# Kernel optimization log

Measured on AMD Instinct MI355X. Metric: run time of the kernel, lower is better.

## Reference

```python
import jax, jax.numpy as jnp
import numpy as np
from jax import lax

V, H, L, F = 50304, 512, 6, 2048
SKIP_INTERVAL = 1
B, S = 4, 1024


def layer_norm(x, w, b, eps=1e-5):
    mu = jnp.mean(x, axis=-1, keepdims=True)
    var = jnp.mean(jnp.square(x - mu), axis=-1, keepdims=True)
    return (x - mu) * lax.rsqrt(var + eps) * w + b


def setup_inputs() -> dict:
    key = jax.random.key(0)
    ks = jax.random.split(key, 8)
    s = 0.02
    return {
        "input_ids": jax.random.randint(ks[0], (B, S), 0, V, dtype=jnp.int64),
        "embed_in": jax.random.normal(ks[1], (V, H), jnp.float32) * s,
        "hp_w": jax.random.normal(ks[2], (H, H), jnp.float32) * s,
        "hp_b": jnp.zeros((H,), jnp.float32),
        "ln_w": jnp.ones((L, H), jnp.float32),
        "ln_b": jnp.zeros((L, H), jnp.float32),
        "W1": jax.random.normal(ks[3], (L, H, F), jnp.float32) * s,
        "b1": jnp.zeros((L, F), jnp.float32),
        "W2": jax.random.normal(ks[4], (L, F, H), jnp.float32) * s,
        "b2": jnp.zeros((L, H), jnp.float32),
        "ln_f_w": jnp.ones((H,), jnp.float32),
        "ln_f_b": jnp.zeros((H,), jnp.float32),
        "embed_out_w": jax.random.normal(ks[5], (V, H), jnp.float32) * s,
    }


def _stack(h, ln_w, ln_b, W1, b1, W2, b2):
    # scan over L layers; each is pre-LN residual MLP: h + gelu(LN(h) @ W1 + b1) @ W2 + b2
    def step(h, p):
        lw, lb, w1, bb1, w2, bb2 = p
        y = layer_norm(h, lw, lb)
        h = h + jnp.dot(jax.nn.gelu(jnp.dot(y, w1) + bb1), w2) + bb2
        return h, None
    h, _ = lax.scan(step, h, (ln_w, ln_b, W1, b1, W2, b2))
    return h


def reference(input_ids, embed_in, hp_w, hp_b, ln_w, ln_b, W1, b1, W2, b2, ln_f_w, ln_f_b, embed_out_w):
    # forward_selective with attention_mask=None and stateless layers is
    # position-independent, so the token loop vectorizes exactly to [B,S,H].
    h = embed_in[input_ids]  # [B,S,H] gather
    h = _stack(h, ln_w, ln_b, W1, b1, W2, b2)
    for _ in range(SKIP_INTERVAL):
        h = jnp.dot(h, hp_w.T) + hp_b  # hidden_proj
        h = _stack(h, ln_w, ln_b, W1, b1, W2, b2)
    normed = layer_norm(h, ln_f_w, ln_f_b)
    logits = jnp.dot(normed, embed_out_w.T)  # [B,S,V]
    final_hidden = h[:, -1, :]  # [B,H]
    return logits, final_hidden
```

## Files before the change

### kernel.cpp

```cpp
#include <hip/hip_runtime.h>
#include <hip/hip_bf16.h>
#include <cstdint>

using bf16 = __hip_bfloat16;
typedef __bf16 bf16x8 __attribute__((ext_vector_type(8)));
typedef float f32x4 __attribute__((ext_vector_type(4)));

constexpr int Hd = 512;
constexpr int Ld = 6;
constexpr int Fd = 2048;
constexpr int Vd = 50304;
constexpr int Vpad = 50432;
constexpr int Md = 4096;

__device__ __forceinline__ unsigned short f2b(float x) {
  return __builtin_bit_cast(unsigned short, __float2bfloat16(x));
}

__device__ __forceinline__ float gelu_tanh(float x) {
  const float c = 0.7978845608028654f;
  float x3 = x * x * x;
  return 0.5f * x * (1.0f + tanhf(c * (x + 0.044715f * x3)));
}

__device__ __forceinline__ void load16_lds(const bf16* g, bf16* l) {
  __builtin_amdgcn_global_load_lds(
      (const __attribute__((address_space(1))) void*)g,
      (__attribute__((address_space(3))) void*)l, 16, 0, 0);
}

__global__ __launch_bounds__(256) void cast8(const float* __restrict__ in,
                                             bf16* __restrict__ out, int n8) {
  int i = blockIdx.x * 256 + threadIdx.x;
  if (i >= n8) return;
  const float4* p = (const float4*)in;
  float4 a = p[2 * i], b = p[2 * i + 1];
  uint4 o = {(unsigned)f2b(a.x) | ((unsigned)f2b(a.y) << 16),
             (unsigned)f2b(a.z) | ((unsigned)f2b(a.w) << 16),
             (unsigned)f2b(b.x) | ((unsigned)f2b(b.y) << 16),
             (unsigned)f2b(b.z) | ((unsigned)f2b(b.w) << 16)};
  ((uint4*)out)[i] = o;
}

__global__ __launch_bounds__(256) void zero16(bf16* __restrict__ p, int n8) {
  int i = blockIdx.x * 256 + threadIdx.x;
  if (i < n8) ((uint4*)p)[i] = uint4{0, 0, 0, 0};
}

__global__ void transpose_cast(const float* __restrict__ in, bf16* __restrict__ out,
                               int R, int C) {
  __shared__ float tile[32][33];
  int l = blockIdx.z;
  in += (size_t)l * R * C;
  out += (size_t)l * R * C;
  int c0 = blockIdx.x * 32, r0 = blockIdx.y * 32;
#pragma unroll
  for (int i = 0; i < 4; i++) {
    int r = r0 + threadIdx.y + i * 8;
    tile[threadIdx.y + i * 8][threadIdx.x] = in[(size_t)r * C + c0 + threadIdx.x];
  }
  __syncthreads();
#pragma unroll
  for (int i = 0; i < 4; i++) {
    int c = c0 + threadIdx.y + i * 8;
    out[(size_t)c * R + r0 + threadIdx.x] = (bf16)tile[threadIdx.x][threadIdx.y + i * 8];
  }
}

__global__ void gather_embed(const int* __restrict__ ids, const float* __restrict__ emb,
                             float* __restrict__ h) {
  int row = blockIdx.x;
  int id = ids[row];
  const float4* src = (const float4*)(emb + (size_t)id * Hd);
  float4* dst = (float4*)(h + (size_t)row * Hd);
  dst[threadIdx.x] = src[threadIdx.x];
}

template <int MODE>
__global__ __launch_bounds__(256) void ln_rows(
    const float* __restrict__ h, const float* __restrict__ p0,
    const float* __restrict__ p1, const float* __restrict__ fb,
    const float* __restrict__ w, const float* __restrict__ b,
    float* __restrict__ hout, bf16* __restrict__ y) {
  int row = blockIdx.x * 4 + (threadIdx.x >> 6);
  int lane = threadIdx.x & 63;
  size_t base = (size_t)row * Hd + lane * 8;
  float xv[8];
  if constexpr (MODE == 0) {
    *(float4*)&xv[0] = *(const float4*)(h + base);
    *(float4*)&xv[4] = *(const float4*)(h + base + 4);
  } else {
    float4 q0 = *(const float4*)(p0 + base), q1 = *(const float4*)(p0 + base + 4);
    float4 r0 = *(const float4*)(p1 + base), r1 = *(const float4*)(p1 + base + 4);
    float4 f0 = *(const float4*)(fb + lane * 8), f1 = *(const float4*)(fb + lane * 8 + 4);
    xv[0] = q0.x + r0.x + f0.x; xv[1] = q0.y + r0.y + f0.y;
    xv[2] = q0.z + r0.z + f0.z; xv[3] = q0.w + r0.w + f0.w;
    xv[4] = q1.x + r1.x + f1.x; xv[5] = q1.y + r1.y + f1.y;
    xv[6] = q1.z + r1.z + f1.z; xv[7] = q1.w + r1.w + f1.w;
    if constexpr (MODE == 1) {
      float4 a0 = *(const float4*)(h + base), a1 = *(const float4*)(h + base + 4);
      xv[0] += a0.x; xv[1] += a0.y; xv[2] += a0.z; xv[3] += a0.w;
      xv[4] += a1.x; xv[5] += a1.y; xv[6] += a1.z; xv[7] += a1.w;
    }
    *(float4*)(hout + base) = make_float4(xv[0], xv[1], xv[2], xv[3]);
    *(float4*)(hout + base + 4) = make_float4(xv[4], xv[5], xv[6], xv[7]);
  }
  float s = 0.f;
#pragma unroll
  for (int j = 0; j < 8; j++) s += xv[j];
#pragma unroll
  for (int off = 1; off < 64; off <<= 1) s += __shfl_xor(s, off);
  float mu = s * (1.0f / 512.0f);
  float s2 = 0.f;
#pragma unroll
  for (int j = 0; j < 8; j++) {
    xv[j] -= mu;
    s2 += xv[j] * xv[j];
  }
#pragma unroll
  for (int off = 1; off < 64; off <<= 1) s2 += __shfl_xor(s2, off);
  float scale = rsqrtf(s2 * (1.0f / 512.0f) + 1e-5f);
  float o[8];
#pragma unroll
  for (int j = 0; j < 8; j++) {
    float wj = w[lane * 8 + j], bj = b[lane * 8 + j];
    o[j] = xv[j] * scale * wj + bj;
  }
  uint4 pk = {(unsigned)f2b(o[0]) | ((unsigned)f2b(o[1]) << 16),
              (unsigned)f2b(o[2]) | ((unsigned)f2b(o[3]) << 16),
              (unsigned)f2b(o[4]) | ((unsigned)f2b(o[5]) << 16),
              (unsigned)f2b(o[6]) | ((unsigned)f2b(o[7]) << 16)};
  *(uint4*)(y + base) = pk;
}

__global__ __launch_bounds__(256) void finish2(
    const float* __restrict__ p0, const float* __restrict__ p1,
    const float* __restrict__ fb, float* __restrict__ h, bf16* __restrict__ hbf) {
  int i = blockIdx.x * 256 + threadIdx.x;
  size_t base = (size_t)i * 8;
  int col = (int)(base & 511);
  float x[8];
#pragma unroll
  for (int j = 0; j < 8; j += 4) {
    float4 a = *(const float4*)(h + base + j);
    float4 q = *(const float4*)(p0 + base + j);
    float4 r = *(const float4*)(p1 + base + j);
    float4 f = *(const float4*)(fb + col + j);
    x[j] = a.x + q.x + r.x + f.x; x[j + 1] = a.y + q.y + r.y + f.y;
    x[j + 2] = a.z + q.z + r.z + f.z; x[j + 3] = a.w + q.w + r.w + f.w;
    *(float4*)(h + base + j) = make_float4(x[j], x[j + 1], x[j + 2], x[j + 3]);
  }
  uint4 pk = {(unsigned)f2b(x[0]) | ((unsigned)f2b(x[1]) << 16),
              (unsigned)f2b(x[2]) | ((unsigned)f2b(x[3]) << 16),
              (unsigned)f2b(x[4]) | ((unsigned)f2b(x[5]) << 16),
              (unsigned)f2b(x[6]) | ((unsigned)f2b(x[7]) << 16)};
  *(uint4*)(hbf + base) = pk;
}


template <int EPI>
__global__ __launch_bounds__(256) void gemm_bt(
    const bf16* __restrict__ A, const bf16* __restrict__ Bt,
    const float* __restrict__ bias, float* __restrict__ outF,
    bf16* __restrict__ outB, int M, int N, int Klen, int lda, int ldb) {
  constexpr int ASZ = 128 * 64;
  constexpr int TILE = 2 * ASZ;
  __shared__ bf16 lds[3 * TILE];
  const int tid = threadIdx.x;
  const int wave = tid >> 6;
  const int lane = tid & 63;
  const int wm = (wave >> 1) * 64;
  const int wn = (wave & 1) * 64;

  const int bn = blockIdx.x;
  const int bm = blockIdx.y;
  const int rowA0 = bm * 128;
  const int rowB0 = bn * 128;
  const int k0 = blockIdx.z * Klen;

  const bf16* srcA[4];
  const bf16* srcB[4];
#pragma unroll
  for (int r = 0; r < 4; r++) {
    int c = r * 256 + tid;
    int row = c >> 3, d = c & 7;
    int cw = d ^ (row & 7);
    srcA[r] = A + (size_t)(rowA0 + row) * lda + k0 + cw * 8;
    srcB[r] = Bt + (size_t)(rowB0 + row) * ldb + k0 + cw * 8;
  }

  f32x4 acc[4][4];
#pragma unroll
  for (int i = 0; i < 4; i++)
#pragma unroll
    for (int j = 0; j < 4; j++) acc[i][j] = (f32x4){0.f, 0.f, 0.f, 0.f};

  const int fr = lane & 15;
  const int hi = lane >> 4;
  const int swz = fr & 7;

  auto STAGE = [&](int slot) {
    bf16* dst = lds + slot * TILE;
#pragma unroll
    for (int r = 0; r < 4; r++) {
      load16_lds(srcA[r], dst + (r * 4 + wave) * 512);
      srcA[r] += 64;
      load16_lds(srcB[r], dst + ASZ + (r * 4 + wave) * 512);
      srcB[r] += 64;
    }
  };

  STAGE(0);
  STAGE(1);
  const int nIter = Klen >> 6;
  int cur = 0, stg = 2;
  for (int it = 0; it < nIter; ++it) {
    if (it < nIter - 1)
      asm volatile("s_waitcnt vmcnt(8)" ::: "memory");
    else
      asm volatile("s_waitcnt vmcnt(0)" ::: "memory");
    __builtin_amdgcn_s_barrier();
    __builtin_amdgcn_sched_barrier(0);
    if (it + 2 < nIter) STAGE(stg);
    const bf16* lA = lds + cur * TILE;
    const bf16* lB = lA + ASZ;
#pragma unroll
    for (int ks = 0; ks < 2; ks++) {
      bf16x8 af[4], bfr[4];
#pragma unroll
      for (int f = 0; f < 4; f++) {
        int rowa = wm + f * 16 + fr;
        af[f] = *(const bf16x8*)(lA + rowa * 64 + ((ks * 4 + hi) ^ swz) * 8);
        int rowb = wn + f * 16 + fr;
        bfr[f] = *(const bf16x8*)(lB + rowb * 64 + ((ks * 4 + hi) ^ swz) * 8);
      }
#pragma unroll
      for (int i = 0; i < 4; i++)
#pragma unroll
        for (int j = 0; j < 4; j++)
          acc[i][j] = __builtin_amdgcn_mfma_f32_16x16x32_bf16(af[i], bfr[j], acc[i][j], 0, 0, 0);
    }
    cur = (cur == 2) ? 0 : cur + 1;
    stg = (stg == 2) ? 0 : stg + 1;
  }

  if constexpr (EPI == 4) outF += (size_t)blockIdx.z * M * N;
  const int orow = hi * 4;
  const int ocol = fr;
#pragma unroll
  for (int i = 0; i < 4; i++) {
#pragma unroll
    for (int j = 0; j < 4; j++) {
      int row0 = rowA0 + wm + i * 16 + orow;
      int col = rowB0 + wn + j * 16 + ocol;
#pragma unroll
      for (int q = 0; q < 4; q++) {
        float v = acc[i][j][q];
        size_t idx = (size_t)(row0 + q) * N + col;
        if constexpr (EPI == 0) {
          outB[idx] = (bf16)gelu_tanh(v + bias[col]);
        } else {
          outF[idx] = v;
        }
      }
    }
  }
}

template <int EPI>
__global__ __launch_bounds__(512) void gemm_bt256(
    const bf16* __restrict__ A, const bf16* __restrict__ Bt,
    const float* __restrict__ bias, float* __restrict__ outF,
    bf16* __restrict__ outB, int M, int N, int lda, int ldb) {
  constexpr int ASZ = 256 * 64;
  constexpr int BSZ = 128 * 64;
  constexpr int TILE = ASZ + BSZ;
  __shared__ bf16 lds[3 * TILE];
  const int tid = threadIdx.x;
  const int wave = tid >> 6;
  const int lane = tid & 63;
  const int wm = (wave >> 1) * 64;
  const int wn = (wave & 1) * 64;

  const int bn = blockIdx.x;
  const int bm = blockIdx.y;
  const int rowA0 = bm * 256;
  const int rowB0 = bn * 128;

  const bf16* srcA[4];
#pragma unroll
  for (int r = 0; r < 4; r++) {
    int c = r * 512 + tid;
    int row = c >> 3, d = c & 7;
    int cw = d ^ (row & 7);
    srcA[r] = A + (size_t)(rowA0 + row) * lda + cw * 8;
  }
  const bf16* srcB[2];
#pragma unroll
  for (int r = 0; r < 2; r++) {
    int c = r * 512 + tid;
    int row = c >> 3, d = c & 7;
    int cw = d ^ (row & 7);
    srcB[r] = Bt + (size_t)(rowB0 + row) * ldb + cw * 8;
  }

  f32x4 acc[4][4];
#pragma unroll
  for (int i = 0; i < 4; i++)
#pragma unroll
    for (int j = 0; j < 4; j++) acc[i][j] = (f32x4){0.f, 0.f, 0.f, 0.f};

  const int fr = lane & 15;
  const int hi = lane >> 4;
  const int swz = fr & 7;

  auto STAGE = [&](int slot) {
    bf16* dst = lds + slot * TILE;
#pragma unroll
    for (int r = 0; r < 4; r++) {
      load16_lds(srcA[r], dst + (r * 8 + wave) * 512);
      srcA[r] += 64;
    }
#pragma unroll
    for (int r = 0; r < 2; r++) {
      load16_lds(srcB[r], dst + ASZ + (r * 8 + wave) * 512);
      srcB[r] += 64;
    }
  };

  STAGE(0);
  STAGE(1);
  const int nIter = 512 >> 6;
  int cur = 0, stg = 2;
  for (int it = 0; it < nIter; ++it) {
    if (it < nIter - 1)
      asm volatile("s_waitcnt vmcnt(6)" ::: "memory");
    else
      asm volatile("s_waitcnt vmcnt(0)" ::: "memory");
    __builtin_amdgcn_s_barrier();
    __builtin_amdgcn_sched_barrier(0);
    if (it + 2 < nIter) STAGE(stg);
    const bf16* lA = lds + cur * TILE;
    const bf16* lB = lA + ASZ;
#pragma unroll
    for (int ks = 0; ks < 2; ks++) {
      bf16x8 af[4], bfr[4];
#pragma unroll
      for (int f = 0; f < 4; f++) {
        int rowa = wm + f * 16 + fr;
        af[f] = *(const bf16x8*)(lA + rowa * 64 + ((ks * 4 + hi) ^ swz) * 8);
        int rowb = wn + f * 16 + fr;
        bfr[f] = *(const bf16x8*)(lB + rowb * 64 + ((ks * 4 + hi) ^ swz) * 8);
      }
#pragma unroll
      for (int i = 0; i < 4; i++)
#pragma unroll
        for (int j = 0; j < 4; j++)
          acc[i][j] = __builtin_amdgcn_mfma_f32_16x16x32_bf16(af[i], bfr[j], acc[i][j], 0, 0, 0);
    }
    cur = (cur == 2) ? 0 : cur + 1;
    stg = (stg == 2) ? 0 : stg + 1;
  }

  const int orow = hi * 4;
  const int ocol = fr;
#pragma unroll
  for (int i = 0; i < 4; i++) {
#pragma unroll
    for (int j = 0; j < 4; j++) {
      int row0 = rowA0 + wm + i * 16 + orow;
      int col = rowB0 + wn + j * 16 + ocol;
#pragma unroll
      for (int q = 0; q < 4; q++) {
        float v = acc[i][j][q];
        size_t idx = (size_t)(row0 + q) * N + col;
        if constexpr (EPI == 0) {
          outB[idx] = (bf16)gelu_tanh(v + bias[col]);
        } else {
          outF[idx] = v;
        }
      }
    }
  }
}

__global__ __launch_bounds__(512, 1) void gemm_logits(
    const bf16* __restrict__ A, const bf16* __restrict__ Bt,
    float* __restrict__ outF, int M, int N, int lda, int ldb) {
  constexpr int ASZ = 256 * 32;
  constexpr int TILE = 2 * ASZ;
  __shared__ bf16 lds[3 * TILE];
  const int tid = threadIdx.x;
  const int wave = tid >> 6;
  const int lane = tid & 63;
  const int wm = (wave >> 2) * 128;
  const int wn = (wave & 3) * 64;

  const int per = gridDim.x >> 3;
  const int wg = (blockIdx.x & 7) * per + (blockIdx.x >> 3);
  const int bm = wg & 15;
  const int bn = wg >> 4;
  const int rowA0 = bm * 256;
  const int rowB0 = bn * 256;

  const bf16* srcA[2];
  const bf16* srcB[2];
#pragma unroll
  for (int r = 0; r < 2; r++) {
    int c = r * 512 + tid;
    int row = c >> 2, d = c & 3;
    int cw = d ^ ((row >> 1) & 3);
    srcA[r] = A + (size_t)(rowA0 + row) * lda + cw * 8;
    srcB[r] = Bt + (size_t)(rowB0 + row) * ldb + cw * 8;
  }

  f32x4 acc[8][4];
#pragma unroll
  for (int i = 0; i < 8; i++)
#pragma unroll
    for (int j = 0; j < 4; j++) acc[i][j] = (f32x4){0.f, 0.f, 0.f, 0.f};

  const int fr = lane & 15;
  const int hi = lane >> 4;
  const int sw32 = (fr >> 1) & 3;

  auto STAGE = [&](int slot) {
    bf16* dst = lds + slot * TILE;
#pragma unroll
    for (int r = 0; r < 2; r++) {
      load16_lds(srcA[r], dst + (r * 8 + wave) * 512);
      srcA[r] += 32;
      load16_lds(srcB[r], dst + ASZ + (r * 8 + wave) * 512);
      srcB[r] += 32;
    }
  };

  STAGE(0);
  STAGE(1);
  const int nIter = 512 >> 5;
  int cur = 0, stg = 2;
  for (int it = 0; it < nIter; ++it) {
    if (it < nIter - 1)
      asm volatile("s_waitcnt vmcnt(4)" ::: "memory");
    else
      asm volatile("s_waitcnt vmcnt(0)" ::: "memory");
    __builtin_amdgcn_s_barrier();
    __builtin_amdgcn_sched_barrier(0);
    if (it + 2 < nIter) STAGE(stg);
    const bf16* lA = lds + cur * TILE;
    const bf16* lB = lA + ASZ;
    bf16x8 af[8], bfr[4];
#pragma unroll
    for (int f = 0; f < 8; f++) {
      int rowa = wm + f * 16 + fr;
      af[f] = *(const bf16x8*)(lA + rowa * 32 + (hi ^ sw32) * 8);
    }
#pragma unroll
    for (int f = 0; f < 4; f++) {
      int rowb = wn + f * 16 + fr;
      bfr[f] = *(const bf16x8*)(lB + rowb * 32 + (hi ^ sw32) * 8);
    }
#pragma unroll
    for (int i = 0; i < 8; i++)
#pragma unroll
      for (int j = 0; j < 4; j++)
        acc[i][j] = __builtin_amdgcn_mfma_f32_16x16x32_bf16(af[i], bfr[j], acc[i][j], 0, 0, 0);
    cur = (cur == 2) ? 0 : cur + 1;
    stg = (stg == 2) ? 0 : stg + 1;
  }

  const int orow = hi * 4;
  const int ocol = fr;
#pragma unroll
  for (int i = 0; i < 8; i++) {
#pragma unroll
    for (int j = 0; j < 4; j++) {
      int row0 = rowA0 + wm + i * 16 + orow;
      int col = rowB0 + wn + j * 16 + ocol;
      if (col < N) {
#pragma unroll
        for (int q = 0; q < 4; q++)
          outF[(size_t)(row0 + q) * N + col] = acc[i][j][q];
      }
    }
  }
}

__global__ void tail_copy(const float* __restrict__ h, float* __restrict__ out) {
  int t = blockIdx.x * 256 + threadIdx.x;
  int b = t >> 9, k = t & 511;
  out[t] = h[((size_t)(b * 1024 + 1023)) * Hd + k];
}

extern "C" void kernel_launch(void* const* d_in, const int* in_sizes, int n_in,
                              void* d_out, int out_size, void* d_ws, size_t ws_size,
                              hipStream_t stream) {
  const int* ids = (const int*)d_in[0];
  const float* emb = (const float*)d_in[1];
  const float* hp_w = (const float*)d_in[2];
  const float* hp_b = (const float*)d_in[3];
  const float* ln_w = (const float*)d_in[4];
  const float* ln_b = (const float*)d_in[5];
  const float* W1 = (const float*)d_in[6];
  const float* b1 = (const float*)d_in[7];
  const float* W2 = (const float*)d_in[8];
  const float* b2 = (const float*)d_in[9];
  const float* lnf_w = (const float*)d_in[10];
  const float* lnf_b = (const float*)d_in[11];
  const float* eow = (const float*)d_in[12];
  float* out = (float*)d_out;

  char* ws = (char*)d_ws;
  float* h = (float*)(ws);
  bf16* ybf = (bf16*)(ws + (8u << 20));
  bf16* abf = (bf16*)(ws + (12u << 20));
  bf16* W1t = (bf16*)(ws + (28u << 20));
  bf16* W2t = (bf16*)(ws + (40u << 20));
  bf16* hpwB = (bf16*)(ws + (52u << 20));
  bf16* eowB = (bf16*)(ws + (53u << 20));

  float* p0 = out;
  float* p1 = out + (size_t)Md * Hd;

  cast8<<<dim3(Vd * Hd / 8 / 256), dim3(256), 0, stream>>>(eow, eowB, Vd * Hd / 8);
  zero16<<<dim3((Vpad - Vd) * Hd / 8 / 256), dim3(256), 0, stream>>>(
      eowB + (size_t)Vd * Hd, (Vpad - Vd) * Hd / 8);
  cast8<<<dim3(Hd * Hd / 8 / 256), dim3(256), 0, stream>>>(hp_w, hpwB, Hd * Hd / 8);
  transpose_cast<<<dim3(Fd / 32, Hd / 32, Ld), dim3(32, 8), 0, stream>>>(W1, W1t, Hd, Fd);
  transpose_cast<<<dim3(Hd / 32, Fd / 32, Ld), dim3(32, 8), 0, stream>>>(W2, W2t, Fd, Hd);

  gather_embed<<<dim3(Md), dim3(128), 0, stream>>>(ids, emb, h);

  auto layer = [&](int l, int mode, const float* fb, const float* lw, const float* lb) {
    if (mode == 0)
      ln_rows<0><<<dim3(Md / 4), dim3(256), 0, stream>>>(h, p0, p1, fb, lw, lb, h, ybf);
    else if (mode == 1)
      ln_rows<1><<<dim3(Md / 4), dim3(256), 0, stream>>>(h, p0, p1, fb, lw, lb, h, ybf);
    else
      ln_rows<2><<<dim3(Md / 4), dim3(256), 0, stream>>>(h, p0, p1, fb, lw, lb, h, ybf);
    gemm_bt256<0><<<dim3(Fd / 128, Md / 256), dim3(512), 0, stream>>>(
        ybf, W1t + (size_t)l * Fd * Hd, b1 + (size_t)l * Fd, (float*)nullptr, abf,
        Md, Fd, Hd, Hd);
    gemm_bt<4><<<dim3(Hd / 128, Md / 128, 2), dim3(256), 0, stream>>>(
        abf, W2t + (size_t)l * Hd * Fd, (const float*)nullptr, p0, (bf16*)nullptr,
        Md, Hd, Fd / 2, Fd, Fd);
  };

  layer(0, 0, nullptr, ln_w, ln_b);
  for (int l = 1; l < Ld; l++)
    layer(l, 1, b2 + (size_t)(l - 1) * Hd, ln_w + (size_t)l * Hd, ln_b + (size_t)l * Hd);
  finish2<<<dim3(Md * Hd / 8 / 256), dim3(256), 0, stream>>>(
      p0, p1, b2 + (size_t)(Ld - 1) * Hd, h, ybf);

  gemm_bt<4><<<dim3(Hd / 128, Md / 128, 2), dim3(256), 0, stream>>>(
      ybf, hpwB, (const float*)nullptr, p0, (bf16*)nullptr, Md, Hd, Hd / 2, Hd, Hd);

  layer(0, 2, hp_b, ln_w, ln_b);
  for (int l = 1; l < Ld; l++)
    layer(l, 1, b2 + (size_t)(l - 1) * Hd, ln_w + (size_t)l * Hd, ln_b + (size_t)l * Hd);

  ln_rows<1><<<dim3(Md / 4), dim3(256), 0, stream>>>(
      h, p0, p1, b2 + (size_t)(Ld - 1) * Hd, lnf_w, lnf_b, h, ybf);
  gemm_logits<<<dim3((Vpad / 256) * (Md / 256)), dim3(512), 0, stream>>>(
      ybf, eowB, out, Md, Vd, Hd, Hd);

  tail_copy<<<dim3(8), dim3(256), 0, stream>>>(h, out + (size_t)Md * Vd);
}
```

Baseline: 944.0 us.

## Use BK=64 double-buffered pipeline in logits GEMM and fuse cast with pad zeroing

The logits GEMM now stages 64-wide K tiles in two LDS buffers instead of 32-wide tiles in three. An 8-way XOR swizzle replaces the old one, and each iteration runs two MFMA sub-steps with a trailing barrier. This halves the number of barrier/wait iterations per tile but gives up one stage of prefetch depth and adds a second barrier per iteration. The vocab weight cast and the pad-row zeroing are merged into one kernel to save a launch.

```diff
diff --git a/kernel.cpp b/kernel.cpp
--- a/kernel.cpp
+++ b/kernel.cpp
@@ -27,6 +27,24 @@
   __builtin_amdgcn_global_load_lds(
       (const __attribute__((address_space(1))) void*)g,
       (__attribute__((address_space(3))) void*)l, 16, 0, 0);
+}
+
+__global__ __launch_bounds__(256) void cast8pad(const float* __restrict__ in,
+                                                bf16* __restrict__ out, int n8cast,
+                                                int n8tot) {
+  int i = blockIdx.x * 256 + threadIdx.x;
+  if (i >= n8tot) return;
+  if (i < n8cast) {
+    const float4* p = (const float4*)in;
+    float4 a = p[2 * i], b = p[2 * i + 1];
+    uint4 o = {(unsigned)f2b(a.x) | ((unsigned)f2b(a.y) << 16),
+               (unsigned)f2b(a.z) | ((unsigned)f2b(a.w) << 16),
+               (unsigned)f2b(b.x) | ((unsigned)f2b(b.y) << 16),
+               (unsigned)f2b(b.z) | ((unsigned)f2b(b.w) << 16)};
+    ((uint4*)out)[i] = o;
+  } else {
+    ((uint4*)out)[i] = uint4{0, 0, 0, 0};
+  }
 }
 
 __global__ __launch_bounds__(256) void cast8(const float* __restrict__ in,
@@ -40,11 +58,6 @@
              (unsigned)f2b(b.x) | ((unsigned)f2b(b.y) << 16),
              (unsigned)f2b(b.z) | ((unsigned)f2b(b.w) << 16)};
   ((uint4*)out)[i] = o;
-}
-
-__global__ __launch_bounds__(256) void zero16(bf16* __restrict__ p, int n8) {
-  int i = blockIdx.x * 256 + threadIdx.x;
-  if (i < n8) ((uint4*)p)[i] = uint4{0, 0, 0, 0};
 }
 
 __global__ void transpose_cast(const float* __restrict__ in, bf16* __restrict__ out,
@@ -387,9 +400,9 @@
 __global__ __launch_bounds__(512, 1) void gemm_logits(
     const bf16* __restrict__ A, const bf16* __restrict__ Bt,
     float* __restrict__ outF, int M, int N, int lda, int ldb) {
-  constexpr int ASZ = 256 * 32;
+  constexpr int ASZ = 256 * 64;
   constexpr int TILE = 2 * ASZ;
-  __shared__ bf16 lds[3 * TILE];
+  __shared__ bf16 lds[2 * TILE];
   const int tid = threadIdx.x;
   const int wave = tid >> 6;
   const int lane = tid & 63;
@@ -403,13 +416,13 @@
   const int rowA0 = bm * 256;
   const int rowB0 = bn * 256;
 
-  const bf16* srcA[2];
-  const bf16* srcB[2];
-#pragma unroll
-  for (int r = 0; r < 2; r++) {
+  const bf16* srcA[4];
+  const bf16* srcB[4];
+#pragma unroll
+  for (int r = 0; r < 4; r++) {
     int c = r * 512 + tid;
-    int row = c >> 2, d = c & 3;
-    int cw = d ^ ((row >> 1) & 3);
+    int row = c >> 3, d = c & 7;
+    int cw = d ^ (row & 7);
     srcA[r] = A + (size_t)(rowA0 + row) * lda + cw * 8;
     srcB[r] = Bt + (size_t)(rowB0 + row) * ldb + cw * 8;
   }
@@ -422,51 +435,52 @@
 
   const int fr = lane & 15;
   const int hi = lane >> 4;
-  const int sw32 = (fr >> 1) & 3;
+  const int swz = fr & 7;
 
   auto STAGE = [&](int slot) {
     bf16* dst = lds + slot * TILE;
 #pragma unroll
-    for (int r = 0; r < 2; r++) {
+    for (int r = 0; r < 4; r++) {
       load16_lds(srcA[r], dst + (r * 8 + wave) * 512);
-      srcA[r] += 32;
+      srcA[r] += 64;
       load16_lds(srcB[r], dst + ASZ + (r * 8 + wave) * 512);
-      srcB[r] += 32;
+      srcB[r] += 64;
     }
   };
 
   STAGE(0);
-  STAGE(1);
-  const int nIter = 512 >> 5;
-  int cur = 0, stg = 2;
+  const int nIter = 512 >> 6;
   for (int it = 0; it < nIter; ++it) {
-    if (it < nIter - 1)
-      asm volatile("s_waitcnt vmcnt(4)" ::: "memory");
+    const int cur = it & 1;
+    if (it + 1 < nIter) STAGE(cur ^ 1);
+    if (it + 1 < nIter)
+      asm volatile("s_waitcnt vmcnt(8)" ::: "memory");
     else
       asm volatile("s_waitcnt vmcnt(0)" ::: "memory");
     __builtin_amdgcn_s_barrier();
     __builtin_amdgcn_sched_barrier(0);
-    if (it + 2 < nIter) STAGE(stg);
     const bf16* lA = lds + cur * TILE;
     const bf16* lB = lA + ASZ;
-    bf16x8 af[8], bfr[4];
-#pragma unroll
-    for (int f = 0; f < 8; f++) {
-      int rowa = wm + f * 16 + fr;
-      af[f] = *(const bf16x8*)(lA + rowa * 32 + (hi ^ sw32) * 8);
-    }
-#pragma unroll
-    for (int f = 0; f < 4; f++) {
-      int rowb = wn + f * 16 + fr;
-      bfr[f] = *(const bf16x8*)(lB + rowb * 32 + (hi ^ sw32) * 8);
-    }
-#pragma unroll
-    for (int i = 0; i < 8; i++)
-#pragma unroll
-      for (int j = 0; j < 4; j++)
-        acc[i][j] = __builtin_amdgcn_mfma_f32_16x16x32_bf16(af[i], bfr[j], acc[i][j], 0, 0, 0);
-    cur = (cur == 2) ? 0 : cur + 1;
-    stg = (stg == 2) ? 0 : stg + 1;
+#pragma unroll
+    for (int ks = 0; ks < 2; ks++) {
+      bf16x8 af[8], bfr[4];
+#pragma unroll
+      for (int f = 0; f < 8; f++) {
+        int rowa = wm + f * 16 + fr;
+        af[f] = *(const bf16x8*)(lA + rowa * 64 + ((ks * 4 + hi) ^ swz) * 8);
+      }
+#pragma unroll
+      for (int f = 0; f < 4; f++) {
+        int rowb = wn + f * 16 + fr;
+        bfr[f] = *(const bf16x8*)(lB + rowb * 64 + ((ks * 4 + hi) ^ swz) * 8);
+      }
+#pragma unroll
+      for (int i = 0; i < 8; i++)
+#pragma unroll
+        for (int j = 0; j < 4; j++)
+          acc[i][j] = __builtin_amdgcn_mfma_f32_16x16x32_bf16(af[i], bfr[j], acc[i][j], 0, 0, 0);
+    }
+    __builtin_amdgcn_s_barrier();
   }
 
   const int orow = hi * 4;
@@ -522,9 +536,10 @@
   float* p0 = out;
   float* p1 = out + (size_t)Md * Hd;
 
-  cast8<<<dim3(Vd * Hd / 8 / 256), dim3(256), 0, stream>>>(eow, eowB, Vd * Hd / 8);
-  zero16<<<dim3((Vpad - Vd) * Hd / 8 / 256), dim3(256), 0, stream>>>(
-      eowB + (size_t)Vd * Hd, (Vpad - Vd) * Hd / 8);
+  {
+    int n8cast = Vd * Hd / 8, n8tot = Vpad * Hd / 8;
+    cast8pad<<<dim3((n8tot + 255) / 256), dim3(256), 0, stream>>>(eow, eowB, n8cast, n8tot);
+  }
   cast8<<<dim3(Hd * Hd / 8 / 256), dim3(256), 0, stream>>>(hp_w, hpwB, Hd * Hd / 8);
   transpose_cast<<<dim3(Fd / 32, Hd / 32, Ld), dim3(32, 8), 0, stream>>>(W1, W1t, Hd, Fd);
   transpose_cast<<<dim3(Hd / 32, Fd / 32, Ld), dim3(32, 8), 0, stream>>>(W2, W2t, Fd, Hd);
```

Measured after the change: 941.2 us. About the same (-0.3%).
